# Kernel optimization log

Hardware: AMD Instinct MI355X
Metric: run time of the kernel (lower is better)

## Reference

```python
import math
import jax, jax.numpy as jnp
import numpy as np
from jax import lax

N_SPIXELS = 1024
N_ITERS = 5


def _layout(H, W, n_spixels):
    # init_grid: regular nw x nh superpixel grid over the image
    nw = int(math.sqrt(n_spixels * W / H))
    nh = int(math.sqrt(n_spixels * H / W))
    S = nw * nh
    sy = (jnp.arange(H) * nh) // H            # [H] superpixel row per pixel row
    sx = (jnp.arange(W) * nw) // W            # [W] superpixel col per pixel col
    idx0 = (sy[:, None] * nw + sx[None, :]).astype(jnp.int32)  # [H,W]
    dy = jnp.array([-1, -1, -1, 0, 0, 0, 1, 1, 1])
    dx = jnp.array([-1, 0, 1, -1, 0, 1, -1, 0, 1])
    ny = sy[None, :, None] + dy[:, None, None]  # [9,H,1]
    nx = sx[None, None, :] + dx[:, None, None]  # [9,1,W]
    valid = (ny >= 0) & (ny < nh) & (nx >= 0) & (nx < nw)        # [9,H,W] (bcast)
    abs_idx = (jnp.clip(ny, 0, nh - 1) * nw + jnp.clip(nx, 0, nw - 1)).astype(jnp.int32)
    abs_idx = jnp.broadcast_to(abs_idx, (9, H, W))
    valid = jnp.broadcast_to(valid, (9, H, W))
    return idx0, abs_idx, valid, S


def _seg_mean(feats, idx_flat, S):
    # feats: [B,C,P] -> per-superpixel mean [B,C,S]
    B, C, P = feats.shape
    data = feats.reshape(B * C, P).T                                   # [P,B*C]
    sums = jax.ops.segment_sum(data, idx_flat, num_segments=S)         # [S,B*C]
    cnt = jax.ops.segment_sum(jnp.ones((P,), feats.dtype), idx_flat, num_segments=S)
    spf = sums / jnp.maximum(cnt, 1e-12)[:, None]
    return spf.T.reshape(B, C, S)


def _forward(feat, w_conv, b_conv):
    B, _, H, W = feat.shape
    x = lax.conv_general_dilated(feat, w_conv, (1, 1), 'SAME',
                                 dimension_numbers=('NCHW', 'OIHW', 'NCHW'))
    featall = jax.nn.relu(x + b_conv[None, :, None, None])  # [B,8,H,W]
    C = featall.shape[1]
    idx0, abs_idx, valid, S = _layout(H, W, N_SPIXELS)
    P = H * W
    # InitSpixelFeats on detached features
    spf = _seg_mean(lax.stop_gradient(featall).reshape(B, C, P), idx0.reshape(P), S)
    idx9 = abs_idx.reshape(9 * P)
    NEG = jnp.asarray(-1e16, featall.dtype)
    Q = None
    for _ in range(N_ITERS):
        # CalcAssoc: negative squared distance to the 9 neighboring superpixels
        spf_g = spf[:, :, abs_idx]                                   # [B,C,9,H,W]
        nd = -jnp.sum((featall[:, :, None] - spf_g) ** 2, axis=1)    # [B,9,H,W]
        nd = jnp.where(valid[None], nd, NEG)
        Q = jax.nn.softmax(nd, axis=1)                               # nd2Q
        # CalcSpixelFeats: weighted scatter-mean of pixel feats into superpixels
        Qm = jnp.where(valid[None], Q, jnp.asarray(0.0, Q.dtype))
        wf = featall[:, :, None, :, :] * Qm[:, None]                 # [B,C,9,H,W]
        num = jax.ops.segment_sum(wf.reshape(B * C, 9 * P).T, idx9, num_segments=S)
        den = jax.ops.segment_sum(Qm.reshape(B, 9 * P).T, idx9, num_segments=S)
        num = num.T.reshape(B, C, S)
        den = den.T[:, None, :]                                      # [B,1,S]
        spf = num / jnp.maximum(den, 1e-12)
    return Q, spf, featall


def setup_inputs():
    key = jax.random.key(0)
    k1, k2, k3 = jax.random.split(key, 3)
    feat = jax.random.normal(k1, (4, 128, 512, 512), jnp.float32)
    w_conv = jax.random.normal(k2, (8, 128, 3, 3), jnp.float32) * 0.02
    b_conv = jnp.zeros((8,), jnp.float32)
    return {"feat": feat, "w_conv": w_conv, "b_conv": b_conv}


def reference(feat, w_conv, b_conv):
    return _forward(feat, w_conv, b_conv)
```

## Files before the change

### kernel.cpp

```cpp
#include <hip/hip_runtime.h>

#define HH 512
#define WW 512
#define NHH 32
#define NWW 32
#define NSP 1024
#define NB 4
#define CIN 128
#define CO 8
#define NITER 5

__global__ __launch_bounds__(256) void conv_relu_kernel(
    const float* __restrict__ feat, const float* __restrict__ wconv,
    const float* __restrict__ bconv, float* __restrict__ featall)
{
    __shared__ float ws[CO * CIN * 9];
    int t = threadIdx.x;
    for (int i = t; i < CO * CIN * 9; i += 256) ws[i] = wconv[i];
    __syncthreads();

    int blk = blockIdx.x;
    int xb = blk & 1;
    int y  = (blk >> 1) & (HH - 1);
    int b  = blk >> 10;
    int x  = xb * 256 + t;

    float acc[CO];
#pragma unroll
    for (int o = 0; o < CO; ++o) acc[o] = 0.f;

    const float* fb = feat + (size_t)b * CIN * HH * WW;
    for (int c = 0; c < CIN; ++c) {
        const float* fc = fb + (size_t)c * HH * WW;
        float v[9];
#pragma unroll
        for (int ky = 0; ky < 3; ++ky) {
            int yy = y + ky - 1;
            bool yok = (yy >= 0) && (yy < HH);
#pragma unroll
            for (int kx = 0; kx < 3; ++kx) {
                int xx = x + kx - 1;
                bool ok = yok && (xx >= 0) && (xx < WW);
                v[ky * 3 + kx] = ok ? fc[(size_t)yy * WW + xx] : 0.f;
            }
        }
#pragma unroll
        for (int o = 0; o < CO; ++o) {
            const float* wc = &ws[(o * CIN + c) * 9];
            float a = acc[o];
#pragma unroll
            for (int k = 0; k < 9; ++k) a = fmaf(v[k], wc[k], a);
            acc[o] = a;
        }
    }
    size_t obase = ((size_t)b * CO) * HH * WW + (size_t)y * WW + x;
#pragma unroll
    for (int o = 0; o < CO; ++o)
        featall[obase + (size_t)o * HH * WW] = fmaxf(acc[o] + bconv[o], 0.f);
}

__global__ __launch_bounds__(256) void init_spf_kernel(
    const float* __restrict__ featall, float* __restrict__ spf)
{
    int blk = blockIdx.x;
    int s = blk & (NSP - 1);
    int b = blk >> 10;
    int sy = s >> 5, sx = s & 31;
    int t = threadIdx.x;
    int ty = t >> 4, tx = t & 15;
    int y = sy * 16 + ty, x = sx * 16 + tx;

    size_t base = ((size_t)b * CO) * HH * WW + (size_t)y * WW + x;
    float f[CO];
#pragma unroll
    for (int c = 0; c < CO; ++c) f[c] = featall[base + (size_t)c * HH * WW];

#pragma unroll
    for (int off = 1; off < 64; off <<= 1)
#pragma unroll
        for (int c = 0; c < CO; ++c) f[c] += __shfl_xor(f[c], off, 64);

    __shared__ float lds[4][CO];
    int wave = t >> 6, lane = t & 63;
    if (lane == 0)
#pragma unroll
        for (int c = 0; c < CO; ++c) lds[wave][c] = f[c];
    __syncthreads();
    if (t < CO) {
        float sum = lds[0][t] + lds[1][t] + lds[2][t] + lds[3][t];
        spf[((size_t)b * CO + t) * NSP + s] = sum * (1.0f / 256.0f);
    }
}

__global__ __launch_bounds__(256) void iter_kernel(
    const float* __restrict__ featall, const float* __restrict__ spf,
    float* __restrict__ num, float* __restrict__ den,
    float* __restrict__ qout, int write_q)
{
    int blk = blockIdx.x;
    int s = blk & (NSP - 1);
    int b = blk >> 10;
    int sy = s >> 5, sx = s & 31;
    int t = threadIdx.x;
    int ty = t >> 4, tx = t & 15;
    int y = sy * 16 + ty, x = sx * 16 + tx;

    int nidx[9]; bool nval[9];
#pragma unroll
    for (int k = 0; k < 9; ++k) {
        int ny = sy + k / 3 - 1;
        int nx = sx + (k % 3) - 1;
        nval[k] = (ny >= 0) && (ny < NHH) && (nx >= 0) && (nx < NWW);
        int cy = min(max(ny, 0), NHH - 1), cx = min(max(nx, 0), NWW - 1);
        nidx[k] = cy * NWW + cx;
    }

    __shared__ float sg[9][CO];
    if (t < 72) {
        int k = t >> 3, c = t & 7;
        sg[k][c] = spf[((size_t)b * CO + c) * NSP + nidx[k]];
    }
    __syncthreads();

    size_t fbase = ((size_t)b * CO) * HH * WW + (size_t)y * WW + x;
    float f[CO];
#pragma unroll
    for (int c = 0; c < CO; ++c) f[c] = featall[fbase + (size_t)c * HH * WW];

    float nd[9];
#pragma unroll
    for (int k = 0; k < 9; ++k) {
        float d = 0.f;
#pragma unroll
        for (int c = 0; c < CO; ++c) { float df = f[c] - sg[k][c]; d = fmaf(df, df, d); }
        nd[k] = -d;
    }
    float m = -1e30f;
#pragma unroll
    for (int k = 0; k < 9; ++k) m = nval[k] ? fmaxf(m, nd[k]) : m;
    float e[9], esum = 0.f;
#pragma unroll
    for (int k = 0; k < 9; ++k) {
        e[k] = nval[k] ? __expf(nd[k] - m) : 0.f;
        esum += e[k];
    }
    float inv = 1.0f / esum;
#pragma unroll
    for (int k = 0; k < 9; ++k) e[k] *= inv;

    if (write_q) {
#pragma unroll
        for (int k = 0; k < 9; ++k)
            qout[(((size_t)b * 9 + k) * HH + y) * WW + x] = e[k];
    }

    __shared__ float red[4][81];
    int lane = t & 63, wave = t >> 6;
#pragma unroll
    for (int k = 0; k < 9; ++k) {
        float v[9];
        v[0] = e[k];
#pragma unroll
        for (int c = 0; c < CO; ++c) v[c + 1] = f[c] * e[k];
#pragma unroll
        for (int off = 1; off < 64; off <<= 1) {
#pragma unroll
            for (int j = 0; j < 9; ++j) v[j] += __shfl_xor(v[j], off, 64);
        }
        if (lane == 0) {
#pragma unroll
            for (int j = 0; j < 9; ++j) red[wave][k * 9 + j] = v[j];
        }
    }
    __syncthreads();
    if (t < 81) {
        int k = t / 9, j = t % 9;
        if (nval[k]) {
            float v = red[0][t] + red[1][t] + red[2][t] + red[3][t];
            if (j == 0) unsafeAtomicAdd(&den[(size_t)b * NSP + nidx[k]], v);
            else        unsafeAtomicAdd(&num[((size_t)b * CO + (j - 1)) * NSP + nidx[k]], v);
        }
    }
}

__global__ __launch_bounds__(256) void update_spf_kernel(
    const float* __restrict__ num, const float* __restrict__ den,
    float* __restrict__ spf_out)
{
    int i = blockIdx.x * 256 + threadIdx.x;
    if (i >= NB * CO * NSP) return;
    int s = i & (NSP - 1);
    int b = (i >> 10) >> 3;
    spf_out[i] = num[i] / fmaxf(den[b * NSP + s], 1e-12f);
}

extern "C" void kernel_launch(void* const* d_in, const int* in_sizes, int n_in,
                              void* d_out, int out_size, void* d_ws, size_t ws_size,
                              hipStream_t stream)
{
    const float* feat  = (const float*)d_in[0];
    const float* wconv = (const float*)d_in[1];
    const float* bconv = (const float*)d_in[2];

    float* out     = (float*)d_out;
    float* qout    = out;
    float* spf_out = out + (size_t)NB * 9 * HH * WW;
    float* featall = spf_out + (size_t)NB * CO * NSP;

    float* spf = (float*)d_ws;
    float* num = spf + (size_t)NB * CO * NSP;
    float* den = num + (size_t)NB * CO * NSP;

    conv_relu_kernel<<<NB * HH * 2, 256, 0, stream>>>(feat, wconv, bconv, featall);
    init_spf_kernel<<<NB * NSP, 256, 0, stream>>>(featall, spf);

    for (int it = 0; it < NITER; ++it) {
        hipMemsetAsync(num, 0, (size_t)(NB * CO * NSP + NB * NSP) * sizeof(float), stream);
        int last = (it == NITER - 1);
        iter_kernel<<<NB * NSP, 256, 0, stream>>>(featall, spf, num, den, qout, last);
        update_spf_kernel<<<(NB * CO * NSP + 255) / 256, 256, 0, stream>>>(
            num, den, last ? spf_out : spf);
    }
}
```

Baseline: 1.666 ms.

## Rewrite 3x3 conv as bf16 MFMA implicit GEMM with LDS-tiled input

Replaces the scalar FP32 direct convolution with an implicit-GEMM kernel. Each block stages a 6x66 input halo tile for 32 channels at a time in LDS, converted to bf16, and issues 16x16x32 bf16 MFMA instructions per tap. The output-channel dimension is padded from 8 to 16, so half of the MFMA work is wasted. Rounding inputs and weights to bf16 lowers precision, which may matter for the softmax association that follows.

```diff
diff --git a/kernel.cpp b/kernel.cpp
--- a/kernel.cpp
+++ b/kernel.cpp
@@ -10,53 +10,97 @@
 #define CO 8
 #define NITER 5
 
-__global__ __launch_bounds__(256) void conv_relu_kernel(
+typedef short bf16x8 __attribute__((ext_vector_type(8)));
+typedef float f32x4 __attribute__((ext_vector_type(4)));
+
+__device__ inline short f2bf(float f) {
+    union { float fv; unsigned u; } v; v.fv = f;
+    unsigned r = v.u + 0x7FFF + ((v.u >> 16) & 1);
+    return (short)(r >> 16);
+}
+
+__global__ __launch_bounds__(256) void conv_mfma_kernel(
     const float* __restrict__ feat, const float* __restrict__ wconv,
     const float* __restrict__ bconv, float* __restrict__ featall)
 {
-    __shared__ float ws[CO * CIN * 9];
-    int t = threadIdx.x;
-    for (int i = t; i < CO * CIN * 9; i += 256) ws[i] = wconv[i];
-    __syncthreads();
-
-    int blk = blockIdx.x;
-    int xb = blk & 1;
-    int y  = (blk >> 1) & (HH - 1);
-    int b  = blk >> 10;
-    int x  = xb * 256 + t;
-
-    float acc[CO];
-#pragma unroll
-    for (int o = 0; o < CO; ++o) acc[o] = 0.f;
-
-    const float* fb = feat + (size_t)b * CIN * HH * WW;
-    for (int c = 0; c < CIN; ++c) {
-        const float* fc = fb + (size_t)c * HH * WW;
-        float v[9];
-#pragma unroll
-        for (int ky = 0; ky < 3; ++ky) {
-            int yy = y + ky - 1;
-            bool yok = (yy >= 0) && (yy < HH);
-#pragma unroll
-            for (int kx = 0; kx < 3; ++kx) {
-                int xx = x + kx - 1;
-                bool ok = yok && (xx >= 0) && (xx < WW);
-                v[ky * 3 + kx] = ok ? fc[(size_t)yy * WW + xx] : 0.f;
+    __shared__ __align__(16) short ldsA[6 * 66 * 40];
+    __shared__ __align__(16) short ldsB[9 * 16 * 32];
+
+    int t  = threadIdx.x;
+    int bx = blockIdx.x & 7;
+    int by = (blockIdx.x >> 3) & 127;
+    int b  = blockIdx.x >> 10;
+
+    for (int i = t; i < 9 * 16 * 32 / 2; i += 256) ((int*)ldsB)[i] = 0;
+
+    int lane = t & 63, w = t >> 6;
+    int row = lane & 15, q = lane >> 4;
+
+    int abase[4];
+#pragma unroll
+    for (int m = 0; m < 4; ++m)
+        abase[m] = ((w * 66 + (m * 16 + row)) * 40 + q * 8) * 2;
+    int bbase = (row * 32 + q * 8) * 2;
+
+    f32x4 acc[4];
+#pragma unroll
+    for (int m = 0; m < 4; ++m) acc[m] = (f32x4)0.f;
+
+    const int c_ld = t >> 3;
+    const int sub  = t & 7;
+
+    for (int chunk = 0; chunk < 4; ++chunk) {
+        int c0 = chunk * 32;
+        __syncthreads();
+        const float* fp = feat + (size_t)(b * CIN + c0 + c_ld) * (HH * WW);
+#pragma unroll
+        for (int yi = 0; yi < 6; ++yi) {
+            int gy = by * 4 + yi - 1;
+            bool yok = (unsigned)gy < HH;
+#pragma unroll
+            for (int i = 0; i < 9; ++i) {
+                int xi = sub * 9 + i;
+                if (xi < 66) {
+                    int gx = bx * 64 + xi - 1;
+                    float v = (yok && (unsigned)gx < WW) ? fp[(size_t)gy * WW + gx] : 0.f;
+                    ldsA[(yi * 66 + xi) * 40 + c_ld] = f2bf(v);
+                }
             }
         }
-#pragma unroll
-        for (int o = 0; o < CO; ++o) {
-            const float* wc = &ws[(o * CIN + c) * 9];
-            float a = acc[o];
-#pragma unroll
-            for (int k = 0; k < 9; ++k) a = fmaf(v[k], wc[k], a);
-            acc[o] = a;
-        }
-    }
-    size_t obase = ((size_t)b * CO) * HH * WW + (size_t)y * WW + x;
-#pragma unroll
-    for (int o = 0; o < CO; ++o)
-        featall[obase + (size_t)o * HH * WW] = fmaxf(acc[o] + bconv[o], 0.f);
+        for (int i = t; i < 9 * 8 * 32; i += 256) {
+            int tap = i >> 8;
+            int o   = (i >> 5) & 7;
+            int c   = i & 31;
+            ldsB[(tap * 16 + o) * 32 + c] = f2bf(wconv[(o * CIN + c0 + c) * 9 + tap]);
+        }
+        __syncthreads();
+
+#pragma unroll
+        for (int tap = 0; tap < 9; ++tap) {
+            bf16x8 bfr = *(const bf16x8*)((const char*)ldsB + bbase + tap * 1024);
+            int ky = tap / 3, kx = tap % 3;
+            int off = (ky * 66 + kx) * 80;
+#pragma unroll
+            for (int m = 0; m < 4; ++m) {
+                bf16x8 afr = *(const bf16x8*)((const char*)ldsA + abase[m] + off);
+                acc[m] = __builtin_amdgcn_mfma_f32_16x16x32_bf16(afr, bfr, acc[m], 0, 0, 0);
+            }
+        }
+    }
+
+    int o = lane & 15;
+    float bias = bconv[o & 7];
+    int y = by * 4 + w;
+#pragma unroll
+    for (int m = 0; m < 4; ++m) {
+#pragma unroll
+        for (int r = 0; r < 4; ++r) {
+            int x = bx * 64 + m * 16 + q * 4 + r;
+            if (o < CO)
+                featall[(((size_t)b * CO + o) * HH + y) * WW + x] =
+                    fmaxf(acc[m][r] + bias, 0.f);
+        }
+    }
 }
 
 __global__ __launch_bounds__(256) void init_spf_kernel(
@@ -211,7 +255,7 @@
     float* num = spf + (size_t)NB * CO * NSP;
     float* den = num + (size_t)NB * CO * NSP;
 
-    conv_relu_kernel<<<NB * HH * 2, 256, 0, stream>>>(feat, wconv, bconv, featall);
+    conv_mfma_kernel<<<NB * 8 * 128, 256, 0, stream>>>(feat, wconv, bconv, featall);
     init_spf_kernel<<<NB * NSP, 256, 0, stream>>>(featall, spf);
 
     for (int it = 0; it < NITER; ++it) {
```

After: 1.486 ms. -10.8%, faster.
